# Kernel tuning notes

Hardware: AMD Instinct MI355X
Metric: run time of the kernel (lower is better)

The kernel has to match this reference:

```python
import jax, jax.numpy as jnp
import numpy as np

N_NODES = 50000


def _gcn_conv(h, W, b, src, dst, dinv):
    # PyG GCNConv: linear transform, then symmetric-normalized sum aggregation
    h = h @ W  # (N, d_out)
    norm = dinv[src] * dinv[dst]  # (E,)
    msg = h[src] * norm[:, None]  # (E, d_out)
    agg = jax.ops.segment_sum(msg, dst, num_segments=N_NODES)
    return agg + b


def setup_inputs() -> dict:
    key = jax.random.key(0)
    ks = jax.random.split(key, 9)
    in_dim, h1, h2, out_dim = 512, 512, 512, 256
    x = jax.random.normal(ks[0], (N_NODES, in_dim), dtype=jnp.float32)
    edge_index = jax.random.randint(ks[1], (2, 800000), 0, N_NODES, dtype=jnp.int64)

    def glorot(k, shape):
        lim = float(np.sqrt(6.0 / (shape[0] + shape[1])))
        return jax.random.uniform(k, shape, jnp.float32, -lim, lim)

    return {
        "x": x,
        "edge_index": edge_index,
        "W1": glorot(ks[2], (in_dim, h1)),
        "b1": jnp.zeros((h1,), jnp.float32),
        "W2": glorot(ks[3], (h1, h2)),
        "b2": jnp.zeros((h2,), jnp.float32),
        "Wout": glorot(ks[4], (h2, out_dim)),
        "bout": jnp.zeros((out_dim,), jnp.float32),
    }


def reference(x, edge_index, W1, b1, W2, b2, Wout, bout):
    # add self-loops (GCNConv default)
    loop = jnp.arange(N_NODES, dtype=edge_index.dtype)
    src = jnp.concatenate([edge_index[0], loop])
    dst = jnp.concatenate([edge_index[1], loop])
    # degree on A + I (target side), deg^{-1/2}
    deg = jax.ops.segment_sum(jnp.ones_like(dst, dtype=x.dtype), dst, num_segments=N_NODES)
    dinv = jnp.where(deg > 0, jax.lax.rsqrt(deg), 0.0)

    h = jax.nn.relu(_gcn_conv(x, W1, b1, src, dst, dinv))
    h = jax.nn.relu(_gcn_conv(h, W2, b2, src, dst, dinv))
    return h @ Wout + bout
```

## Files before the change

### kernel.cpp

```cpp
#include <hip/hip_runtime.h>

#define NN 50000
#define MP 50048
#define DD 512
#define EE 800000
#define NSCAN 196
#define SCB 3321
#define G1TILES 1564

typedef unsigned short u16;
typedef __attribute__((ext_vector_type(4))) float f32x4;
typedef __attribute__((ext_vector_type(8))) __bf16 bf16x8;
typedef __attribute__((ext_vector_type(8))) short s16x8;

typedef __attribute__((address_space(1))) const void GVoid;
typedef __attribute__((address_space(3))) void LVoid;

__device__ __forceinline__ u16 f2bf(float f) {
  union { float f; unsigned u; } x; x.f = f;
  unsigned r = x.u + 0x7fffu + ((x.u >> 16) & 1u);
  return (u16)(r >> 16);
}
__device__ __forceinline__ float bf2f(u16 b) {
  union { unsigned u; float f; } x; x.u = ((unsigned)b) << 16;
  return x.f;
}


__global__ __launch_bounds__(256) void setup_k(int* __restrict__ cnt,
                                               const float* __restrict__ W1, u16* __restrict__ W1T,
                                               const float* __restrict__ W2, u16* __restrict__ W2T,
                                               const float* __restrict__ Wo, u16* __restrict__ WoT) {
  const int b = (int)blockIdx.x, t = threadIdx.x;
  if (b < 196) { int i = b * 256 + t; if (i < NN) cnt[i] = 1; return; }
  const float* W; u16* WT; int ncols, idx;
  if (b < 1220)      { W = W1; WT = W1T; ncols = 512; idx = (b - 196) * 256 + t; }
  else if (b < 2244) { W = W2; WT = W2T; ncols = 512; idx = (b - 1220) * 256 + t; }
  else               { W = Wo; WT = WoT; ncols = 256; idx = (b - 2244) * 256 + t; }
  if (idx >= 512 * ncols) return;
  int n = idx >> 9, k = idx & 511;
  WT[idx] = f2bf(W[(size_t)k * ncols + n]);
}

__global__ __launch_bounds__(256) void count_k(const int* __restrict__ dst, int* __restrict__ cnt) {
  int e = blockIdx.x * 256 + threadIdx.x;
  if (e < EE) atomicAdd(&cnt[dst[e]], 1);
}


__global__ __launch_bounds__(256) void scan1_k(const int* __restrict__ cnt, int* __restrict__ bsum) {
  __shared__ int s[256];
  const int t = threadIdx.x;
  const int i = blockIdx.x * 256 + t;
  s[t] = (i < NN) ? cnt[i] : 0;
  __syncthreads();
  for (int off = 128; off > 0; off >>= 1) {
    if (t < off) s[t] += s[t + off];
    __syncthreads();
  }
  if (t == 0) bsum[blockIdx.x] = s[0];
}

__global__ __launch_bounds__(256) void scan2_k(const int* __restrict__ bsum, int* __restrict__ boff) {
  __shared__ int s[256];
  const int t = threadIdx.x;
  const int v = (t < NSCAN) ? bsum[t] : 0;
  s[t] = v;
  __syncthreads();
  for (int off = 1; off < 256; off <<= 1) {
    int a = s[t];
    int b = (t >= off) ? s[t - off] : 0;
    __syncthreads();
    s[t] = a + b;
    __syncthreads();
  }
  if (t < NSCAN) boff[t] = s[t] - v;
}

__global__ __launch_bounds__(256) void scan3_k(const int* __restrict__ cnt, const int* __restrict__ boff,
                                               int* __restrict__ rowp, int* __restrict__ cursor,
                                               float* __restrict__ dinv) {
  __shared__ int s[256];
  const int t = threadIdx.x;
  const int i = blockIdx.x * 256 + t;
  const int v = (i < NN) ? cnt[i] : 0;
  s[t] = v;
  __syncthreads();
  for (int off = 1; off < 256; off <<= 1) {
    int a = s[t];
    int b = (t >= off) ? s[t - off] : 0;
    __syncthreads();
    s[t] = a + b;
    __syncthreads();
  }
  const int excl = s[t] - v + boff[blockIdx.x];
  if (i < NN) {
    rowp[i] = excl; cursor[i] = excl;
    dinv[i] = rsqrtf((float)v);
  }
  if (i == NN - 1) rowp[NN] = excl + v;
}


__global__ __launch_bounds__(256) void gemm1_k(const float* __restrict__ X, const u16* __restrict__ BT,
                                               u16* __restrict__ C,
                                               const int* __restrict__ src, const int* __restrict__ dst,
                                               const float* __restrict__ dinv, int* __restrict__ cursor,
                                               int2* __restrict__ csr) {
  __shared__ u16 As[2][128 * 32];
  __shared__ u16 Bs[2][128 * 32];
  const int t = threadIdx.x;

  if (blockIdx.x < SCB) {
    int e = (int)blockIdx.x * 256 + t;
    if (e < EE) {
      int d = dst[e], sn = src[e];
      int pos = atomicAdd(&cursor[d], 1);
      csr[pos] = make_int2(sn, __float_as_int(dinv[sn] * dinv[d]));
    } else if (e < EE + NN) {
      int i = e - EE;
      int pos = atomicAdd(&cursor[i], 1);
      float di = dinv[i];
      csr[pos] = make_int2(i, __float_as_int(di * di));
    }
    return;
  }

  const int g = (int)blockIdx.x - SCB;
  const int xcd = g & 7;
  const int idx = g >> 3;
  const int q = G1TILES >> 3, r = G1TILES & 7;
  const int tile = (xcd < r ? xcd * (q + 1) : r * (q + 1) + (xcd - r) * q) + idx;
  const int bm = tile >> 2;
  const int bn = tile & 3;

  const int lane = t & 63;
  const int wc = (t >> 6) & 1;
  const int wr = (t >> 7) & 1;
  f32x4 acc[4][4] = {};
  const int r0 = t >> 2;
  const int kc = (t & 3) * 8;
  const int row1 = bm * 128 + 64 + r0;
  const float* Xp0 = X + (size_t)(bm * 128 + r0) * DD + kc;
  const float* Xp1 = X + (size_t)(row1 < NN ? row1 : NN - 1) * DD + kc;
  const u16* Bb = BT + (size_t)bn * 128 * DD + (size_t)r0 * DD + kc;

  f32x4 a0, a1, a2, a3;
  auto loadA = [&](int kt) {
    a0 = *(const f32x4*)(Xp0 + kt);
    a1 = *(const f32x4*)(Xp0 + kt + 4);
    a2 = *(const f32x4*)(Xp1 + kt);
    a3 = *(const f32x4*)(Xp1 + kt + 4);
  };
  auto writeA = [&](int buf) {
    bf16x8 w0, w1;
    #pragma unroll
    for (int j = 0; j < 4; ++j) {
      w0[j] = (__bf16)a0[j]; w0[4 + j] = (__bf16)a1[j];
      w1[j] = (__bf16)a2[j]; w1[4 + j] = (__bf16)a3[j];
    }
    *(bf16x8*)&As[buf][t * 8] = w0;
    *(bf16x8*)&As[buf][2048 + t * 8] = w1;
  };
  auto stageB = [&](int buf, int kt) {
    __builtin_amdgcn_global_load_lds((GVoid*)(Bb + kt),           (LVoid*)(&Bs[buf][t * 8]),        16, 0, 0);
    __builtin_amdgcn_global_load_lds((GVoid*)(Bb + 64 * DD + kt), (LVoid*)(&Bs[buf][2048 + t * 8]), 16, 0, 0);
  };

  loadA(0);
  stageB(0, 0);
  writeA(0);
  __syncthreads();

  #pragma unroll 2
  for (int step = 0; step < 16; ++step) {
    const int cur = step & 1;
    if (step < 15) { loadA((step + 1) * 32); stageB(cur ^ 1, (step + 1) * 32); }
    bf16x8 af[4], bv[4];
    #pragma unroll
    for (int m = 0; m < 4; ++m)
      af[m] = *(const bf16x8*)&As[cur][(wr * 64 + m * 16 + (lane & 15)) * 32 + (lane >> 4) * 8];
    #pragma unroll
    for (int n = 0; n < 4; ++n)
      bv[n] = *(const bf16x8*)&Bs[cur][(wc * 64 + n * 16 + (lane & 15)) * 32 + (lane >> 4) * 8];
    #pragma unroll
    for (int m = 0; m < 4; ++m) {
      #pragma unroll
      for (int n = 0; n < 4; ++n)
        acc[m][n] = __builtin_amdgcn_mfma_f32_16x16x32_bf16(af[m], bv[n], acc[m][n], 0, 0, 0);
    }
    if (step < 15) writeA(cur ^ 1);
    __syncthreads();
  }

  const int rb = bm * 128 + wr * 64 + ((lane >> 4) * 4);
  const int cb = bn * 128 + wc * 64 + (lane & 15);
  #pragma unroll
  for (int m = 0; m < 4; ++m) {
    #pragma unroll
    for (int rr = 0; rr < 4; ++rr) {
      const int row = rb + m * 16 + rr;
      if (row < NN) {
        #pragma unroll
        for (int n = 0; n < 4; ++n)
          C[(size_t)row * 512 + cb + n * 16] = f2bf(acc[m][n][rr]);
      }
    }
  }
}


template<int OUT_BF16>
__global__ __launch_bounds__(256) void gemm_k(const u16* __restrict__ A, const u16* __restrict__ BT,
                                              void* __restrict__ Cv, const float* __restrict__ bias,
                                              int M, int N) {
  const int nwg = (int)gridDim.x;
  const int id = (int)blockIdx.x;
  const int xcd = id & 7;
  const int idx = id >> 3;
  const int q = nwg >> 3, r = nwg & 7;
  const int tile = (xcd < r ? xcd * (q + 1) : r * (q + 1) + (xcd - r) * q) + idx;
  const int ntn = N >> 7;
  const int bm = tile / ntn;
  const int bn = tile % ntn;

  __shared__ u16 As[2][128 * 32];
  __shared__ u16 Bs[2][128 * 32];
  const int t = threadIdx.x;
  const int lane = t & 63;
  const int wc = (t >> 6) & 1;
  const int wr = (t >> 7) & 1;
  f32x4 acc[4][4] = {};
  const int r0 = t >> 2;
  const int kc = (t & 3) * 8;
  const u16* Ab = A + (size_t)bm * 128 * DD + (size_t)r0 * DD + kc;
  const u16* Bb = BT + (size_t)bn * 128 * DD + (size_t)r0 * DD + kc;

  auto stage = [&](int buf, int kt) {
    __builtin_amdgcn_global_load_lds((GVoid*)(Ab + kt),           (LVoid*)(&As[buf][t * 8]),        16, 0, 0);
    __builtin_amdgcn_global_load_lds((GVoid*)(Ab + 64 * DD + kt), (LVoid*)(&As[buf][2048 + t * 8]), 16, 0, 0);
    __builtin_amdgcn_global_load_lds((GVoid*)(Bb + kt),           (LVoid*)(&Bs[buf][t * 8]),        16, 0, 0);
    __builtin_amdgcn_global_load_lds((GVoid*)(Bb + 64 * DD + kt), (LVoid*)(&Bs[buf][2048 + t * 8]), 16, 0, 0);
  };

  stage(0, 0);
  __syncthreads();

  #pragma unroll 2
  for (int step = 0; step < 16; ++step) {
    const int cur = step & 1;
    if (step < 15) stage(cur ^ 1, (step + 1) * 32);
    bf16x8 af[4], bv[4];
    #pragma unroll
    for (int m = 0; m < 4; ++m)
      af[m] = *(const bf16x8*)&As[cur][(wr * 64 + m * 16 + (lane & 15)) * 32 + (lane >> 4) * 8];
    #pragma unroll
    for (int n = 0; n < 4; ++n)
      bv[n] = *(const bf16x8*)&Bs[cur][(wc * 64 + n * 16 + (lane & 15)) * 32 + (lane >> 4) * 8];
    #pragma unroll
    for (int m = 0; m < 4; ++m) {
      #pragma unroll
      for (int n = 0; n < 4; ++n)
        acc[m][n] = __builtin_amdgcn_mfma_f32_16x16x32_bf16(af[m], bv[n], acc[m][n], 0, 0, 0);
    }
    __syncthreads();
  }

  const int rb = bm * 128 + wr * 64 + ((lane >> 4) * 4);
  const int cb = bn * 128 + wc * 64 + (lane & 15);
  #pragma unroll
  for (int m = 0; m < 4; ++m) {
    #pragma unroll
    for (int rr = 0; rr < 4; ++rr) {
      const int row = rb + m * 16 + rr;
      if (row < M) {
        #pragma unroll
        for (int n = 0; n < 4; ++n) {
          const int col = cb + n * 16;
          float v = acc[m][n][rr];
          if (bias) v += bias[col];
          if (OUT_BF16) ((u16*)Cv)[(size_t)row * N + col] = f2bf(v);
          else          ((float*)Cv)[(size_t)row * N + col] = v;
        }
      }
    }
  }
}


__global__ __launch_bounds__(256) void aggregate_k(const u16* __restrict__ H, const int* __restrict__ rowp,
                                                   const int2* __restrict__ csr,
                                                   const float* __restrict__ bias,
                                                   u16* __restrict__ out) {
  const int wid = threadIdx.x >> 6;
  const int lane = threadIdx.x & 63;
  const int node = blockIdx.x * 4 + wid;
  const int d0 = lane * 8;
  const int beg = rowp[node];
  const int end = rowp[node + 1];
  float acc[8] = {0.f, 0.f, 0.f, 0.f, 0.f, 0.f, 0.f, 0.f};
  int e = beg;
  for (; e + 4 <= end; e += 4) {
    const int2 c0 = csr[e], c1 = csr[e + 1], c2 = csr[e + 2], c3 = csr[e + 3];
    const s16x8 v0 = *(const s16x8*)(H + (size_t)c0.x * DD + d0);
    const s16x8 v1 = *(const s16x8*)(H + (size_t)c1.x * DD + d0);
    const s16x8 v2 = *(const s16x8*)(H + (size_t)c2.x * DD + d0);
    const s16x8 v3 = *(const s16x8*)(H + (size_t)c3.x * DD + d0);
    const float w0 = __int_as_float(c0.y), w1 = __int_as_float(c1.y);
    const float w2 = __int_as_float(c2.y), w3 = __int_as_float(c3.y);
    #pragma unroll
    for (int j = 0; j < 8; ++j) {
      acc[j] += bf2f((u16)v0[j]) * w0;
      acc[j] += bf2f((u16)v1[j]) * w1;
      acc[j] += bf2f((u16)v2[j]) * w2;
      acc[j] += bf2f((u16)v3[j]) * w3;
    }
  }
  for (; e < end; ++e) {
    const int2 c = csr[e];
    const s16x8 v = *(const s16x8*)(H + (size_t)c.x * DD + d0);
    const float w = __int_as_float(c.y);
    #pragma unroll
    for (int j = 0; j < 8; ++j) acc[j] += bf2f((u16)v[j]) * w;
  }
  s16x8 o;
  #pragma unroll
  for (int j = 0; j < 8; ++j) {
    float r = acc[j] + bias[d0 + j];
    r = fmaxf(r, 0.f);
    o[j] = (short)f2bf(r);
  }
  *(s16x8*)(out + (size_t)node * DD + d0) = o;
}


extern "C" void kernel_launch(void* const* d_in, const int* in_sizes, int n_in,
                              void* d_out, int out_size, void* d_ws, size_t ws_size,
                              hipStream_t stream) {
  const float* x    = (const float*)d_in[0];
  const int*   ei   = (const int*)d_in[1];
  const float* W1   = (const float*)d_in[2];
  const float* b1   = (const float*)d_in[3];
  const float* W2   = (const float*)d_in[4];
  const float* b2   = (const float*)d_in[5];
  const float* Wout = (const float*)d_in[6];
  const float* bout = (const float*)d_in[7];
  float* out = (float*)d_out;
  (void)in_sizes; (void)n_in; (void)out_size; (void)ws_size;

  char* ws = (char*)d_ws;
  size_t off = 0;
  auto alloc = [&](size_t bytes) -> char* {
    char* p = ws + off;
    off = (off + bytes + 255) & ~(size_t)255;
    return p;
  };
  u16*   xb   = (u16*)alloc((size_t)MP * DD * 2);
  u16*   H    = (u16*)alloc((size_t)NN * DD * 2);
  u16*   W1T  = (u16*)alloc(512 * 512 * 2);
  u16*   W2T  = (u16*)alloc(512 * 512 * 2);
  u16*   WoT  = (u16*)alloc(256 * 512 * 2);
  int*   cnt  = (int*)alloc(NN * 4);
  float* dinv = (float*)alloc(NN * 4);
  int*   rowp = (int*)alloc((NN + 1) * 4);
  int*   cur  = (int*)alloc(NN * 4);
  int2*  csr  = (int2*)alloc((size_t)(EE + NN) * 8);
  int*   bsum = (int*)alloc(NSCAN * 4);
  int*   boff = (int*)alloc(NSCAN * 4);

  const int* srcp = ei;
  const int* dstp = ei + EE;

  setup_k<<<2756, 256, 0, stream>>>(cnt, W1, W1T, W2, W2T, Wout, WoT);
  count_k<<<(EE + 255) / 256, 256, 0, stream>>>(dstp, cnt);
  scan1_k<<<NSCAN, 256, 0, stream>>>(cnt, bsum);
  scan2_k<<<1, 256, 0, stream>>>(bsum, boff);
  scan3_k<<<NSCAN, 256, 0, stream>>>(cnt, boff, rowp, cur, dinv);

  gemm1_k<<<SCB + G1TILES, 256, 0, stream>>>(x, W1T, H, srcp, dstp, dinv, cur, csr);
  aggregate_k<<<NN / 4, 256, 0, stream>>>(H, rowp, csr, b1, xb);
  gemm_k<1><<<(MP / 128) * (512 / 128), 256, 0, stream>>>(xb, W2T, (void*)H, nullptr, NN, 512);
  aggregate_k<<<NN / 4, 256, 0, stream>>>(H, rowp, csr, b2, xb);
  gemm_k<0><<<(MP / 128) * (256 / 128), 256, 0, stream>>>(xb, WoT, (void*)out, bout, NN, 256);
}
```

Baseline: 478.6 us.

## Split aggregation across feature slices and edge groups with cross-lane reduction

The aggregation kernel now splits each node's 512-wide feature row into 8 slices, one block per slice, and within a wavefront processes 4 edges in parallel (16 lanes per edge, 4 bf16 features per lane). Partial sums are combined with xor shuffles and one lane group writes the result. The aim is more memory-level parallelism and better latency hiding for the irregular gather, at the cost of 8x more blocks, redundant rowp/csr reads per slice, and narrower 8-byte loads instead of 16-byte loads.

```diff
diff --git a/kernel.cpp b/kernel.cpp
--- a/kernel.cpp
+++ b/kernel.cpp
@@ -12,6 +12,7 @@
 typedef __attribute__((ext_vector_type(4))) float f32x4;
 typedef __attribute__((ext_vector_type(8))) __bf16 bf16x8;
 typedef __attribute__((ext_vector_type(8))) short s16x8;
+typedef __attribute__((ext_vector_type(4))) short s16x4;
 
 typedef __attribute__((address_space(1))) const void GVoid;
 typedef __attribute__((address_space(3))) void LVoid;
@@ -292,45 +293,41 @@
                                                    const int2* __restrict__ csr,
                                                    const float* __restrict__ bias,
                                                    u16* __restrict__ out) {
+  const int slice = (int)blockIdx.x & 7;
+  const int grp = (int)blockIdx.x >> 3;
   const int wid = threadIdx.x >> 6;
   const int lane = threadIdx.x & 63;
-  const int node = blockIdx.x * 4 + wid;
-  const int d0 = lane * 8;
+  const int g = lane >> 4;
+  const int l = lane & 15;
+  const int node = grp * 4 + wid;
+  const int d0 = slice * 64 + l * 4;
   const int beg = rowp[node];
   const int end = rowp[node + 1];
-  float acc[8] = {0.f, 0.f, 0.f, 0.f, 0.f, 0.f, 0.f, 0.f};
-  int e = beg;
-  for (; e + 4 <= end; e += 4) {
-    const int2 c0 = csr[e], c1 = csr[e + 1], c2 = csr[e + 2], c3 = csr[e + 3];
-    const s16x8 v0 = *(const s16x8*)(H + (size_t)c0.x * DD + d0);
-    const s16x8 v1 = *(const s16x8*)(H + (size_t)c1.x * DD + d0);
-    const s16x8 v2 = *(const s16x8*)(H + (size_t)c2.x * DD + d0);
-    const s16x8 v3 = *(const s16x8*)(H + (size_t)c3.x * DD + d0);
-    const float w0 = __int_as_float(c0.y), w1 = __int_as_float(c1.y);
-    const float w2 = __int_as_float(c2.y), w3 = __int_as_float(c3.y);
-    #pragma unroll
-    for (int j = 0; j < 8; ++j) {
-      acc[j] += bf2f((u16)v0[j]) * w0;
-      acc[j] += bf2f((u16)v1[j]) * w1;
-      acc[j] += bf2f((u16)v2[j]) * w2;
-      acc[j] += bf2f((u16)v3[j]) * w3;
-    }
-  }
-  for (; e < end; ++e) {
-    const int2 c = csr[e];
-    const s16x8 v = *(const s16x8*)(H + (size_t)c.x * DD + d0);
+  const u16* Hd = H + d0;
+  float a0 = 0.f, a1 = 0.f, a2 = 0.f, a3 = 0.f;
+  for (int e = beg + g; ; e += 4) {
+    if (__builtin_amdgcn_ballot_w64(e < end) == 0ull) break;
+    const bool ok = e < end;
+    const int2 c = ok ? csr[e] : make_int2(node, 0);
     const float w = __int_as_float(c.y);
-    #pragma unroll
-    for (int j = 0; j < 8; ++j) acc[j] += bf2f((u16)v[j]) * w;
-  }
-  s16x8 o;
-  #pragma unroll
-  for (int j = 0; j < 8; ++j) {
-    float r = acc[j] + bias[d0 + j];
-    r = fmaxf(r, 0.f);
-    o[j] = (short)f2bf(r);
-  }
-  *(s16x8*)(out + (size_t)node * DD + d0) = o;
+    const s16x4 v = *(const s16x4*)(Hd + (size_t)c.x * DD);
+    a0 += bf2f((u16)v[0]) * w;
+    a1 += bf2f((u16)v[1]) * w;
+    a2 += bf2f((u16)v[2]) * w;
+    a3 += bf2f((u16)v[3]) * w;
+  }
+  a0 += __shfl_xor(a0, 16); a0 += __shfl_xor(a0, 32);
+  a1 += __shfl_xor(a1, 16); a1 += __shfl_xor(a1, 32);
+  a2 += __shfl_xor(a2, 16); a2 += __shfl_xor(a2, 32);
+  a3 += __shfl_xor(a3, 16); a3 += __shfl_xor(a3, 32);
+  if (g == 0) {
+    s16x4 o;
+    o[0] = (short)f2bf(fmaxf(a0 + bias[d0 + 0], 0.f));
+    o[1] = (short)f2bf(fmaxf(a1 + bias[d0 + 1], 0.f));
+    o[2] = (short)f2bf(fmaxf(a2 + bias[d0 + 2], 0.f));
+    o[3] = (short)f2bf(fmaxf(a3 + bias[d0 + 3], 0.f));
+    *(s16x4*)(out + (size_t)node * DD + d0) = o;
+  }
 }
 
 
@@ -377,9 +374,11 @@
   scan2_k<<<1, 256, 0, stream>>>(bsum, boff);
   scan3_k<<<NSCAN, 256, 0, stream>>>(cnt, boff, rowp, cur, dinv);
 
+  const int agg_grid = (NN / 4) * 8;
+
   gemm1_k<<<SCB + G1TILES, 256, 0, stream>>>(x, W1T, H, srcp, dstp, dinv, cur, csr);
-  aggregate_k<<<NN / 4, 256, 0, stream>>>(H, rowp, csr, b1, xb);
+  aggregate_k<<<agg_grid, 256, 0, stream>>>(H, rowp, csr, b1, xb);
   gemm_k<1><<<(MP / 128) * (512 / 128), 256, 0, stream>>>(xb, W2T, (void*)H, nullptr, NN, 512);
-  aggregate_k<<<NN / 4, 256, 0, stream>>>(H, rowp, csr, b2, xb);
+  aggregate_k<<<agg_grid, 256, 0, stream>>>(H, rowp, csr, b2, xb);
   gemm_k<0><<<(MP / 128) * (256 / 128), 256, 0, stream>>>(xb, WoT, (void*)out, bout, NN, 256);
 }
```

New measurement: 692.1 us. 1.45x slower.
